# Kernel optimization log

Measured on AMD Instinct MI355X. Metric: run time of the kernel, lower is better.

The kernel has to match this reference:

```python
import jax, jax.numpy as jnp
from jax import lax
import numpy as np

B, H, W = 8, 1024, 1024
NUM_POINTS = 10
THRESHOLD_RATIO = 0.5
K_PEAKS = 512  # cap on peak candidates fed to greedy NMS


def setup_inputs() -> dict:
    key = jax.random.key(0)
    ks = jax.random.split(key, 8)
    return {
        "rgb_image": jax.random.uniform(ks[0], (B, 3, H, W), jnp.float32),
        "depth_image": jax.random.uniform(ks[1], (B, 1, H, W), jnp.float32),
        "conv1_w": jax.random.normal(ks[2], (32, 12, 3, 3), jnp.float32) * 0.1,
        "conv1_b": jax.random.normal(ks[3], (32,), jnp.float32) * 0.1,
        "bn_gamma": jnp.ones((32,), jnp.float32),
        "bn_beta": jnp.zeros((32,), jnp.float32),
        "bn_mean": jax.random.normal(ks[4], (32,), jnp.float32) * 0.1,
        "bn_var": jax.random.uniform(ks[5], (32,), jnp.float32) + 0.5,
        "conv2_w": jax.random.normal(ks[6], (1, 32, 1, 1), jnp.float32) * 0.1,
        "conv2_b": jnp.zeros((1,), jnp.float32),
    }


def dwt2(x):
    # Haar DWT exactly as in the torch module (row split then column split)
    x01 = x[..., 0::2, :] * 0.5
    x02 = x[..., 1::2, :] * 0.5
    LL = x01[..., 0::2] + x02[..., 0::2]
    LH = x01[..., 0::2] - x02[..., 0::2]
    HL = x01[..., 1::2] + x02[..., 1::2]
    HH = x01[..., 1::2] - x02[..., 1::2]
    return LL, LH, HL, HH


def conv2d(x, w, b=None, pad=0, groups=1):
    y = lax.conv_general_dilated(x, w, (1, 1), [(pad, pad), (pad, pad)],
                                 dimension_numbers=("NCHW", "OIHW", "NCHW"),
                                 feature_group_count=groups)
    if b is not None:
        y = y + b[None, :, None, None]
    return y


def gaussian_smooth(x, k=5, sigma=1.0):
    ax = jnp.arange(-(k // 2), k // 2 + 1, dtype=jnp.float32)
    xx, yy = jnp.meshgrid(ax, ax, indexing="ij")
    ker = jnp.exp(-(xx ** 2 + yy ** 2) / (2.0 * sigma ** 2))
    ker = ker / ker.sum()
    C = x.shape[1]
    wk = jnp.tile(ker[None, None], (C, 1, 1, 1))  # depthwise
    return conv2d(x, wk, pad=k // 2, groups=C)


def find_points(s):
    """Greedy spatial-NMS peak picking on a single (h,w) saliency map.
    Returns (NUM_POINTS, 2) normalized (x, y) coords."""
    h, w = s.shape
    min_dist = float(max(max(h, w) // 20, 20))
    flat = s.reshape(-1)
    mp = lax.reduce_window(s, -jnp.inf, lax.max, (3, 3), (1, 1), [(1, 1), (1, 1)])
    peak_flat = ((s == mp) & (s > 0)).reshape(-1)
    peak_scores = jnp.where(peak_flat, flat, -jnp.inf)
    top_vals, top_idx = lax.top_k(peak_scores, K_PEAKS)  # sorted desc = torch argsort
    valid = top_vals > -jnp.inf
    px = (top_idx % w).astype(jnp.float32)
    py = (top_idx // w).astype(jnp.float32)
    pc = jnp.stack([px, py], axis=-1)                     # (K,2)
    dist = jnp.sqrt(((pc[:, None, :] - pc[None, :, :]) ** 2).sum(-1))  # (K,K)
    ar = jnp.arange(K_PEAKS)

    def body(i, st):
        avail, sel, cnt = st
        take = avail[i] & valid[i] & (cnt < NUM_POINTS)
        sel = sel.at[i].set(take)
        suppress = (dist[i] < min_dist) & (ar > i)  # nearby[:i+1]=False in torch
        avail = jnp.where(take, avail & (~suppress), avail)
        return avail, sel, cnt + take.astype(jnp.int32)

    _, sel, n_chosen = lax.fori_loop(
        0, K_PEAKS, body,
        (jnp.ones(K_PEAKS, bool), jnp.zeros(K_PEAKS, bool), jnp.int32(0)))

    # compact chosen peak indices (in descending-score order) into first slots
    pos = jnp.cumsum(sel.astype(jnp.int32)) - 1
    scatter_pos = jnp.where(sel, pos, NUM_POINTS)  # out-of-range -> dropped
    buf = jnp.zeros(NUM_POINTS, jnp.int32).at[scatter_pos].set(top_idx, mode="drop")
    # fallback: top saliency excluding all peaks (matches torch fill-up branch)
    fb_scores = jnp.where(peak_flat, -jnp.inf, flat)
    _, fb_idx = lax.top_k(fb_scores, NUM_POINTS)
    slot = jnp.arange(NUM_POINTS)
    fb = fb_idx[jnp.clip(slot - n_chosen, 0, NUM_POINTS - 1)]
    sel_idx = jnp.where(slot < n_chosen, buf, fb)
    cx = (sel_idx % w).astype(jnp.float32) / w
    cy = (sel_idx // w).astype(jnp.float32) / h
    return jnp.stack([cx, cy], axis=-1)


def boxes_from_mask(masks):
    binm = masks[:, 0] > THRESHOLD_RATIO  # (B,H,W)
    Hh, Ww = binm.shape[1], binm.shape[2]
    rows = binm.any(axis=2)
    cols = binm.any(axis=1)
    ri = jnp.arange(Hh)
    ci = jnp.arange(Ww)
    rmin = jnp.min(jnp.where(rows, ri[None, :], Hh), axis=1)
    rmax = jnp.max(jnp.where(rows, ri[None, :], -1), axis=1)
    cmin = jnp.min(jnp.where(cols, ci[None, :], Ww), axis=1)
    cmax = jnp.max(jnp.where(cols, ci[None, :], -1), axis=1)
    has = rows.any(axis=1)
    boxes = jnp.stack([cmin, rmin, cmax, rmax], axis=-1).astype(jnp.float32)
    default = jnp.array([0.0, 0.0, Ww - 1.0, Hh - 1.0], jnp.float32)
    return jnp.where(has[:, None], boxes, default[None, :])


def reference(rgb_image, depth_image, conv1_w, conv1_b, bn_gamma, bn_beta,
              bn_mean, bn_var, conv2_w, conv2_b):
    rgb_gray = rgb_image.mean(axis=1, keepdims=True)
    rLL, rLH, rHL, rHH = dwt2(rgb_gray)
    dLL, dLH, dHL, dHH = dwt2(depth_image)
    E_rgb = jnp.sqrt(rLH ** 2 + rHL ** 2 + rHH ** 2 + 1e-8)
    E_depth = jnp.sqrt(dLH ** 2 + dHL ** 2 + dHH ** 2 + 1e-8)
    E_rgb_s = gaussian_smooth(E_rgb)
    E_depth_s = gaussian_smooth(E_depth)
    freq = jnp.concatenate(
        [rLL, rLH, rHL, rHH, dLL, dLH, dHL, dHH, E_rgb, E_depth, E_rgb_s, E_depth_s],
        axis=1)  # (B,12,H/2,W/2)
    x = conv2d(freq, conv1_w, conv1_b, pad=1)
    inv = lax.rsqrt(bn_var + 1e-5)
    x = bn_gamma[None, :, None, None] * (x - bn_mean[None, :, None, None]) * inv[None, :, None, None] + bn_beta[None, :, None, None]
    x = jax.nn.gelu(x)
    sal = jax.nn.sigmoid(conv2d(x, conv2_w, conv2_b))  # (B,1,H/2,W/2)
    masks = jax.image.resize(sal, (sal.shape[0], 1, H, W), method="bilinear")
    coords = jax.vmap(find_points)(sal[:, 0])          # (B,N,2)
    labels = jnp.ones((sal.shape[0], NUM_POINTS), jnp.int32)
    boxes = boxes_from_mask(masks)                     # (B,4)
    return coords, labels, boxes, masks
```

## Files before the change

kernel.cpp:

```cpp
#include <hip/hip_runtime.h>
#include <math.h>


#define CHW 262144
#define FULLHW 1048576
#define NB1 64
#define NB2 32
#define PROW 514
#define PREC (514*514)

typedef __attribute__((ext_vector_type(8))) short bf16x8;
typedef __attribute__((ext_vector_type(16))) float f32x16;

static __device__ __forceinline__ unsigned short f2bf(float x) {
  unsigned u = __float_as_uint(x);
  u += 0x7FFFu + ((u >> 16) & 1u);
  return (unsigned short)(u >> 16);
}
static __device__ __forceinline__ float bf2f(unsigned short h) {
  return __uint_as_float(((unsigned)h) << 16);
}

static constexpr size_t OFF_SAL   = 0;
static constexpr size_t OFF_THR   = 8388608;
static constexpr size_t OFF_CNT   = OFF_THR + 256;
static constexpr size_t OFF_CAND  = OFF_CNT + 256;
static constexpr size_t OFF_PART  = OFF_CAND + 131072;
static constexpr size_t OFF_APACK = OFF_PART + 32768;
static constexpr size_t OFF_EP    = OFF_APACK + 20480;
static constexpr size_t OFF_PKM   = OFF_EP + 512;
static constexpr size_t OFF_DYN   = OFF_PKM + 2097152;

static constexpr int SDY[9] = {-1,-1,-1, 0,0,0, 1,1,1};
static constexpr int SDX[9] = {-1, 0, 1,-1,0,1,-1,0,1};

__global__ void k_init(unsigned* __restrict__ cnt,
                       const float* __restrict__ w1, const float* __restrict__ b1,
                       const float* __restrict__ gam, const float* __restrict__ bet,
                       const float* __restrict__ mean, const float* __restrict__ var,
                       const float* __restrict__ w2, const float* __restrict__ b2,
                       unsigned short* __restrict__ apack, float* __restrict__ ep) {
  int i = blockIdx.x * 256 + threadIdx.x;
  if (i < 16) cnt[i] = 0;
  if (i < 9216) {
    int e = i & 7, lane = (i >> 3) & 63, frag = i >> 9;
    int s = frag >> 1, hh = frag & 1;
    int co = lane & 31;
    int c = ((lane >> 5) << 3) + e;
    float val = (c < 12) ? w1[co * 108 + c * 9 + s] : 0.0f;
    unsigned short hb = f2bf(val);
    apack[i] = hh ? f2bf(val - bf2f(hb)) : hb;
  }
  if (i < 96) {
    int t = i >> 5, rem = i & 31, kg = rem >> 4, reg = rem & 15;
    int co = (reg & 3) + 8 * (reg >> 2) + 4 * kg;
    float sc = gam[co] * rsqrtf(var[co] + 1e-5f);
    float v = (t == 0) ? sc
            : (t == 1) ? (b1[co] - mean[co]) * sc + bet[co]
                       : w2[co];
    ep[i] = v;
  } else if (i == 96) {
    ep[96] = b2[0];
  }
}

__global__ __launch_bounds__(256) void k_zero(unsigned short* __restrict__ freq2) {
  int i = blockIdx.x * 256 + threadIdx.x;
  int bi = blockIdx.y;
  if (i >= 8208) return;
  int q = i & 1, r = (i >> 1) % 2052, pl = (i >> 1) / 2052;
  int row, col;
  if (r < 514)        { row = 0;   col = r; }
  else if (r < 1028)  { row = 513; col = r - 514; }
  else if (r < 1540)  { row = r - 1028 + 1; col = 0; }
  else                { row = r - 1540 + 1; col = 513; }
  size_t off = ((size_t)(bi * 2 + pl) * PREC + (size_t)row * PROW + col) * 16;
  uint4* p = (uint4*)(freq2 + off) + q;
  *p = make_uint4(0u, 0u, 0u, 0u);
}

__global__ __launch_bounds__(256) void k_freq(const float* __restrict__ rgb,
                                              const float* __restrict__ dep,
                                              unsigned short* __restrict__ freq2,
                                              float* __restrict__ ebuf, int b0) {
  int t = blockIdx.x * 256 + threadIdx.x;
  int bi = blockIdx.y;
  int b = b0 + bi;
  int xp = t & 255, y = t >> 8;
  const float* base = rgb + (size_t)b * 3 * FULLHW + (size_t)(2 * y) * 1024 + 4 * xp;
  float4 R0 = *(const float4*)(base);
  float4 R1 = *(const float4*)(base + 1024);
  float4 G0 = *(const float4*)(base + FULLHW);
  float4 G1 = *(const float4*)(base + FULLHW + 1024);
  float4 Bl0 = *(const float4*)(base + 2 * FULLHW);
  float4 Bl1 = *(const float4*)(base + 2 * FULLHW + 1024);
  const float* dbase = dep + (size_t)b * FULLHW + (size_t)(2 * y) * 1024 + 4 * xp;
  float4 D0 = *(const float4*)(dbase);
  float4 D1 = *(const float4*)(dbase + 1024);

  float gt[4], gb[4], dt[4], db_[4];
  gt[0] = (R0.x + G0.x + Bl0.x) / 3.0f; gt[1] = (R0.y + G0.y + Bl0.y) / 3.0f;
  gt[2] = (R0.z + G0.z + Bl0.z) / 3.0f; gt[3] = (R0.w + G0.w + Bl0.w) / 3.0f;
  gb[0] = (R1.x + G1.x + Bl1.x) / 3.0f; gb[1] = (R1.y + G1.y + Bl1.y) / 3.0f;
  gb[2] = (R1.z + G1.z + Bl1.z) / 3.0f; gb[3] = (R1.w + G1.w + Bl1.w) / 3.0f;
  dt[0] = D0.x; dt[1] = D0.y; dt[2] = D0.z; dt[3] = D0.w;
  db_[0] = D1.x; db_[1] = D1.y; db_[2] = D1.z; db_[3] = D1.w;

  unsigned short hs[2][8], ls[2][8];
  float er[2], ed[2];
  #pragma unroll
  for (int j = 0; j < 2; ++j) {
    float a = gt[2 * j] * 0.5f, bb = gb[2 * j] * 0.5f;
    float c = gt[2 * j + 1] * 0.5f, d = gb[2 * j + 1] * 0.5f;
    float v[8];
    v[0] = a + bb; v[1] = a - bb; v[2] = c + d; v[3] = c - d;
    float da = dt[2 * j] * 0.5f, db2 = db_[2 * j] * 0.5f;
    float dc = dt[2 * j + 1] * 0.5f, dd = db_[2 * j + 1] * 0.5f;
    v[4] = da + db2; v[5] = da - db2; v[6] = dc + dd; v[7] = dc - dd;
    er[j] = sqrtf(v[1] * v[1] + v[2] * v[2] + v[3] * v[3] + 1e-8f);
    ed[j] = sqrtf(v[5] * v[5] + v[6] * v[6] + v[7] * v[7] + 1e-8f);
    #pragma unroll
    for (int cc = 0; cc < 8; ++cc) {
      unsigned short hb = f2bf(v[cc]);
      hs[j][cc] = hb;
      ls[j][cc] = f2bf(v[cc] - bf2f(hb));
    }
  }
  unsigned short* dst = freq2 +
      ((size_t)(bi * 2) * PREC + (size_t)(y + 1) * PROW + (2 * xp + 1)) * 16;
  uint4* d4 = (uint4*)dst;
  d4[0] = ((const uint4*)hs[0])[0]; d4[1] = ((const uint4*)ls[0])[0];
  d4[2] = ((const uint4*)hs[1])[0]; d4[3] = ((const uint4*)ls[1])[0];
  float* eb = ebuf + (size_t)bi * 2 * CHW + (size_t)y * 512 + 2 * xp;
  *(float2*)(eb) = make_float2(er[0], er[1]);
  *(float2*)(eb + CHW) = make_float2(ed[0], ed[1]);
}

__constant__ float GW[25] = {
  0.00296901f, 0.01330621f, 0.02193824f, 0.01330621f, 0.00296901f,
  0.01330621f, 0.05963435f, 0.09832035f, 0.05963435f, 0.01330621f,
  0.02193824f, 0.09832035f, 0.16210276f, 0.09832035f, 0.02193824f,
  0.01330621f, 0.05963435f, 0.09832035f, 0.05963435f, 0.01330621f,
  0.00296901f, 0.01330621f, 0.02193824f, 0.01330621f, 0.00296901f};

__global__ __launch_bounds__(256) void k_smooth(const float* __restrict__ ebuf,
                                                unsigned short* __restrict__ freq2) {
  int t = blockIdx.x * 256 + threadIdx.x;
  int bi = blockIdx.y;
  int x = t & 511, y = t >> 9;
  const float* eb = ebuf + (size_t)bi * 2 * CHW;
  float accv[2];
  #pragma unroll
  for (int ch = 0; ch < 2; ++ch) {
    const float* fin = eb + ch * CHW;
    float acc = 0.0f;
    #pragma unroll
    for (int i = 0; i < 5; ++i) {
      int yy = y + i - 2;
      if (yy < 0 || yy > 511) continue;
      #pragma unroll
      for (int j = 0; j < 5; ++j) {
        int xx = x + j - 2;
        if (xx < 0 || xx > 511) continue;
        acc += GW[i * 5 + j] * fin[yy * 512 + xx];
      }
    }
    accv[ch] = acc;
  }
  float erc = eb[t], edc = eb[CHW + t];
  unsigned short rec[16];
  float v4[4] = {erc, edc, accv[0], accv[1]};
  #pragma unroll
  for (int j = 0; j < 4; ++j) {
    unsigned short hb = f2bf(v4[j]);
    rec[j] = hb;
    rec[8 + j] = f2bf(v4[j] - bf2f(hb));
  }
  #pragma unroll
  for (int j = 4; j < 8; ++j) { rec[j] = 0; rec[8 + j] = 0; }
  unsigned short* px = freq2 +
      ((size_t)(bi * 2 + 1) * PREC + (size_t)(y + 1) * PROW + (x + 1)) * 16;
  ((uint4*)px)[0] = ((const uint4*)rec)[0];
  ((uint4*)px)[1] = ((const uint4*)rec)[1];
}

__global__ __launch_bounds__(256) void k_conv(const unsigned short* __restrict__ freq2,
    const unsigned short* __restrict__ apack, const float* __restrict__ ep,
    float* __restrict__ sal, int b0) {
  int tid = threadIdx.x;
  int l = tid & 63, wv = tid >> 6;
  int y = blockIdx.y;
  int xw = blockIdx.x * 128 + wv * 32;
  int bi = blockIdx.z;
  int n = l & 31, kg = l >> 5;

  const unsigned short* pb0 = freq2 +
      ((size_t)(bi * 2 + kg) * PREC + (size_t)(y + 1) * PROW + (xw + n + 1)) * 16;
  const unsigned short* ab = apack + l * 8;

  bf16x8 Bh[9], Bl[9];
  #pragma unroll
  for (int s = 0; s < 9; ++s) {
    const int doff = (SDY[s] * PROW + SDX[s]) * 16;
    Bh[s] = *(const bf16x8*)(pb0 + doff);
    Bl[s] = *(const bf16x8*)(pb0 + doff + 8);
  }

  f32x16 acc = {};
  #pragma unroll
  for (int s = 0; s < 9; ++s) {
    bf16x8 Ah = *(const bf16x8*)(ab + s * 1024);
    bf16x8 Al = *(const bf16x8*)(ab + s * 1024 + 512);
    acc = __builtin_amdgcn_mfma_f32_32x32x16_bf16(Ah, Bh[s], acc, 0, 0, 0);
    acc = __builtin_amdgcn_mfma_f32_32x32x16_bf16(Al, Bh[s], acc, 0, 0, 0);
    acc = __builtin_amdgcn_mfma_f32_32x32x16_bf16(Ah, Bl[s], acc, 0, 0, 0);
  }

  const float* e0 = ep + kg * 16;
  const float* e1 = ep + 32 + kg * 16;
  const float* e2 = ep + 64 + kg * 16;
  float s2 = 0.0f;
  #pragma unroll
  for (int r = 0; r < 16; ++r) {
    float t = acc[r] * e0[r] + e1[r];
    float z = t * (1.5957691216057308f + 0.07135481283247183f * (t * t));
    s2 += (t / (1.0f + __expf(-z))) * e2[r];
  }
  s2 += __shfl_xor(s2, 32);
  s2 += ep[96];
  float res = 1.0f / (1.0f + __expf(-s2));
  if (l < 32)
    sal[(size_t)(b0 + bi) * CHW + (size_t)y * 512 + xw + n] = res;
}

__global__ __launch_bounds__(256) void k_resize(const float* __restrict__ sal,
                                                float* __restrict__ masks,
                                                int* __restrict__ part) {
  int b = blockIdx.y;
  int blk = blockIdx.x;
  int t = threadIdx.x;
  const float* sp = sal + (size_t)b * CHW;
  float* mp = masks + (size_t)b * FULLHW;
  int mnX = 0x7FFFFFFF, mxX = -1, mnY = 0x7FFFFFFF, mxY = -1;
  int c0 = 4 * t;
  #pragma unroll
  for (int r = 0; r < 4; ++r) {
    int Y = blk * 4 + r;
    int y0 = (Y - 1) >> 1;
    float wy = (Y & 1) ? 0.25f : 0.75f;
    int y0c = y0 < 0 ? 0 : y0, y1c = (y0 + 1 > 511) ? 511 : y0 + 1;
    const float* r0 = sp + y0c * 512;
    const float* r1 = sp + y1c * 512;
    float o[4];
    #pragma unroll
    for (int j = 0; j < 4; ++j) {
      int X = c0 + j;
      int x0 = (X - 1) >> 1;
      float wx = (X & 1) ? 0.25f : 0.75f;
      int x0c = x0 < 0 ? 0 : x0, x1c = (x0 + 1 > 511) ? 511 : x0 + 1;
      float v00 = r0[x0c], v01 = r0[x1c], v10 = r1[x0c], v11 = r1[x1c];
      o[j] = (1.0f - wy) * ((1.0f - wx) * v00 + wx * v01)
           + wy * ((1.0f - wx) * v10 + wx * v11);
      if (o[j] > 0.5f) {
        mnX = min(mnX, X); mxX = max(mxX, X);
        mnY = min(mnY, Y); mxY = max(mxY, Y);
      }
    }
    *(float4*)(mp + (size_t)Y * 1024 + c0) = make_float4(o[0], o[1], o[2], o[3]);
  }
  __shared__ int s0[256], s1[256], s2[256], s3[256];
  s0[t] = mnX; s1[t] = mxX; s2[t] = mnY; s3[t] = mxY;
  __syncthreads();
  for (int off = 128; off > 0; off >>= 1) {
    if (t < off) {
      s0[t] = min(s0[t], s0[t + off]); s1[t] = max(s1[t], s1[t + off]);
      s2[t] = min(s2[t], s2[t + off]); s3[t] = max(s3[t], s3[t + off]);
    }
    __syncthreads();
  }
  if (t == 0) {
    int* pp = part + (b * 256 + blk) * 4;
    pp[0] = s0[0]; pp[1] = s1[0]; pp[2] = s2[0]; pp[3] = s3[0];
  }
}

__global__ __launch_bounds__(256) void k_boxreduce(const int* __restrict__ part,
                                                   float* __restrict__ out) {
  int b = blockIdx.x, t = threadIdx.x;
  const int* pp = part + (b * 256 + t) * 4;
  __shared__ int s0[256], s1[256], s2[256], s3[256];
  s0[t] = pp[0]; s1[t] = pp[1]; s2[t] = pp[2]; s3[t] = pp[3];
  __syncthreads();
  for (int off = 128; off > 0; off >>= 1) {
    if (t < off) {
      s0[t] = min(s0[t], s0[t + off]); s1[t] = max(s1[t], s1[t + off]);
      s2[t] = min(s2[t], s2[t + off]); s3[t] = max(s3[t], s3[t + off]);
    }
    __syncthreads();
  }
  if (t == 0) {
    float x0, y0, x1, y1;
    if (s3[0] < 0) { x0 = 0.0f; y0 = 0.0f; x1 = 1023.0f; y1 = 1023.0f; }
    else { x0 = (float)s0[0]; y0 = (float)s2[0]; x1 = (float)s1[0]; y1 = (float)s3[0]; }
    out[240 + b * 4 + 0] = x0;
    out[240 + b * 4 + 1] = y0;
    out[240 + b * 4 + 2] = x1;
    out[240 + b * 4 + 3] = y1;
  }
}

__global__ __launch_bounds__(256) void k_hist1(const float* __restrict__ sal,
                                               unsigned* __restrict__ h1p,
                                               unsigned char* __restrict__ pkm) {
  __shared__ unsigned sH[4096];
  int b = blockIdx.y, tid = threadIdx.x;
  for (int i = tid; i < 4096; i += 256) sH[i] = 0;
  __syncthreads();
  const float* sp = sal + (size_t)b * CHW;
  int base = blockIdx.x * 4096;
  for (int it = 0; it < 4; ++it) {
    int p = base + it * 1024 + tid * 4;
    int x0 = p & 511, y = p >> 9;
    int ym = (y > 0) ? y - 1 : 0, yp = (y < 511) ? y + 1 : 511;
    const float* r0 = sp + ym * 512;
    const float* r1 = sp + y * 512;
    const float* r2 = sp + yp * 512;
    float4 m0 = *(const float4*)(r0 + x0);
    float4 m1 = *(const float4*)(r1 + x0);
    float4 m2 = *(const float4*)(r2 + x0);
    float l0 = x0 ? r0[x0 - 1] : m0.x;
    float l1 = x0 ? r1[x0 - 1] : m1.x;
    float l2 = x0 ? r2[x0 - 1] : m2.x;
    float q0 = (x0 < 508) ? r0[x0 + 4] : m0.w;
    float q1 = (x0 < 508) ? r1[x0 + 4] : m1.w;
    float q2 = (x0 < 508) ? r2[x0 + 4] : m2.w;
    float a0[6] = {l0, m0.x, m0.y, m0.z, m0.w, q0};
    float a1[6] = {l1, m1.x, m1.y, m1.z, m1.w, q1};
    float a2[6] = {l2, m2.x, m2.y, m2.z, m2.w, q2};
    unsigned pw = 0;
    #pragma unroll
    for (int j = 0; j < 4; ++j) {
      float r0m = fmaxf(fmaxf(a0[j], a0[j + 1]), a0[j + 2]);
      float r1m = fmaxf(fmaxf(a1[j], a1[j + 1]), a1[j + 2]);
      float r2m = fmaxf(fmaxf(a2[j], a2[j + 1]), a2[j + 2]);
      float cmax = fmaxf(fmaxf(r0m, r1m), r2m);
      float sv = a1[j + 1];
      bool pk = (sv > 0.0f) && (sv >= cmax);
      pw |= (pk ? 1u : 0u) << (8 * j);
      unsigned bin = (__float_as_uint(sv) >> 21) & 2047;
      atomicAdd(&sH[(pk ? 0 : 2048) + bin], 1u);
    }
    *(unsigned*)(pkm + (size_t)b * CHW + p) = pw;
  }
  __syncthreads();
  unsigned* dst = h1p + ((size_t)b * NB1 + blockIdx.x) * 4096;
  for (int i = tid; i < 4096; i += 256) dst[i] = sH[i];
}

__global__ __launch_bounds__(256) void k_scan(const unsigned* __restrict__ hp,
                                              int* __restrict__ thr, int level,
                                              int np) {
  int c = blockIdx.x, b = blockIdx.y, t = threadIdx.x;
  __shared__ unsigned sBins[2048];
  __shared__ unsigned sS[256];
  __shared__ int sT;
  unsigned bv[8] = {0, 0, 0, 0, 0, 0, 0, 0};
  for (int p = 0; p < np; ++p) {
    const unsigned* q = hp + ((size_t)(b * np + p)) * 4096 + c * 2048 + t * 8;
    uint4 a = *(const uint4*)(q);
    uint4 d = *(const uint4*)(q + 4);
    bv[0] += a.x; bv[1] += a.y; bv[2] += a.z; bv[3] += a.w;
    bv[4] += d.x; bv[5] += d.y; bv[6] += d.z; bv[7] += d.w;
  }
  unsigned part = 0;
  #pragma unroll
  for (int r = 0; r < 8; ++r) {
    sBins[t * 8 + r] = bv[r];
    part += bv[r];
  }
  sS[t] = part;
  __syncthreads();
  for (int off = 1; off < 256; off <<= 1) {
    unsigned add = (t + off < 256) ? sS[t + off] : 0;
    __syncthreads();
    sS[t] += add;
    __syncthreads();
  }
  int K = (c == 0) ? 512 : 10;
  int* tb = thr + (c * 8 + b) * 4;
  if (level == 1) { K -= tb[1]; if (K < 1) K = 1; }
  if (t == 0) sT = -1;
  __syncthreads();
  if (sS[t] >= (unsigned)K && (t == 255 || sS[t + 1] < (unsigned)K)) sT = t;
  __syncthreads();
  if (t == 0) {
    int T = 0;
    unsigned run = 0;
    if (sT >= 0) {
      int ts = sT;
      run = (ts < 255) ? sS[ts + 1] : 0;
      for (int r = 7; r >= 0; --r) {
        unsigned v = sBins[ts * 8 + r];
        run += v;
        if (run >= (unsigned)K) { T = ts * 8 + r; run -= v; break; }
      }
    } else {
      T = 0;
      run = sS[0] - sBins[0];
    }
    if (level == 0) { tb[0] = T; tb[1] = (int)run; }
    else           { tb[2] = (tb[0] << 11) | T; }
  }
}

__global__ __launch_bounds__(256) void k_hist2(const float* __restrict__ sal,
                                               const unsigned char* __restrict__ pkm,
                                               const int* __restrict__ thr,
                                               unsigned* __restrict__ h2p) {
  __shared__ unsigned sH[4096];
  int b = blockIdx.y, tid = threadIdx.x;
  for (int i = tid; i < 4096; i += 256) sH[i] = 0;
  __syncthreads();
  int t0 = thr[(0 * 8 + b) * 4];
  int t1 = thr[(1 * 8 + b) * 4];
  const float* sp = sal + (size_t)b * CHW;
  const unsigned char* pp = pkm + (size_t)b * CHW;
  int base = blockIdx.x * 8192;
  for (int it = 0; it < 8; ++it) {
    int p = base + it * 1024 + tid * 4;
    float4 s4 = *(const float4*)(sp + p);
    unsigned pk4 = *(const unsigned*)(pp + p);
    float sv[4] = {s4.x, s4.y, s4.z, s4.w};
    #pragma unroll
    for (int j = 0; j < 4; ++j) {
      bool pk = ((pk4 >> (8 * j)) & 255u) != 0;
      unsigned bits = __float_as_uint(sv[j]);
      int tt = pk ? t0 : t1;
      if ((int)(bits >> 21) == tt)
        atomicAdd(&sH[(pk ? 0 : 2048) + ((bits >> 10) & 2047)], 1u);
    }
  }
  __syncthreads();
  unsigned* dst = h2p + ((size_t)b * NB2 + blockIdx.x) * 4096;
  for (int i = tid; i < 4096; i += 256) dst[i] = sH[i];
}

__global__ __launch_bounds__(256) void k_compact(const float* __restrict__ sal,
                                                 const unsigned char* __restrict__ pkm,
                                                 const int* __restrict__ thr,
                                                 unsigned* __restrict__ cnt,
                                                 unsigned long long* __restrict__ cand) {
  int b = blockIdx.y;
  int p = (blockIdx.x * 256 + threadIdx.x) * 4;
  const float* sp = sal + (size_t)b * CHW;
  float4 s4 = *(const float4*)(sp + p);
  unsigned pk4 = *(const unsigned*)(pkm + (size_t)b * CHW + p);
  unsigned q0 = (unsigned)thr[(0 * 8 + b) * 4 + 2];
  unsigned q1 = (unsigned)thr[(1 * 8 + b) * 4 + 2];
  float sv[4] = {s4.x, s4.y, s4.z, s4.w};
  #pragma unroll
  for (int j = 0; j < 4; ++j) {
    bool pk = ((pk4 >> (8 * j)) & 255u) != 0;
    unsigned bits = __float_as_uint(sv[j]);
    unsigned q = pk ? q0 : q1;
    int c = pk ? 0 : 1;
    if ((bits >> 10) >= q) {
      unsigned pos = atomicAdd(&cnt[c * 8 + b], 1u);
      if (pos < 1024)
        cand[((size_t)(c * 8 + b) << 10) + pos] =
            ((unsigned long long)bits << 32) | (unsigned)(~(p + j));
    }
  }
}

__device__ inline void bitonic1024_desc(unsigned long long* sKey) {
  int t = threadIdx.x;
  for (unsigned k = 2; k <= 1024; k <<= 1) {
    for (unsigned j = k >> 1; j > 0; j >>= 1) {
      __syncthreads();
      #pragma unroll
      for (int e = 0; e < 2; ++e) {
        unsigned i = (unsigned)t + (unsigned)e * 512u;
        unsigned l = i ^ j;
        if (l > i) {
          unsigned long long a = sKey[i], bb = sKey[l];
          if (((i & k) == 0) ? (a < bb) : (a > bb)) { sKey[i] = bb; sKey[l] = a; }
        }
      }
    }
  }
  __syncthreads();
}

__global__ __launch_bounds__(512) void k_nms(const unsigned long long* __restrict__ cand,
                                             const unsigned* __restrict__ cnt,
                                             float* __restrict__ out) {
  __shared__ unsigned long long sKey[1024];
  __shared__ unsigned sIdx[512];
  __shared__ int sAvail[512];
  __shared__ int sSel[16];
  int b = blockIdx.x, t = threadIdx.x;
  if (t < 10) out[160 + b * 10 + t] = 1.0f;
  int Cp = (int)cnt[b]; if (Cp > 1024) Cp = 1024;
  const unsigned long long* cp = cand + ((size_t)b << 10);
  sKey[t] = (t < Cp) ? cp[t] : 0ULL;
  sKey[t + 512] = (t + 512 < Cp) ? cp[t + 512] : 0ULL;
  bitonic1024_desc(sKey);
  sIdx[t] = (unsigned)(~sKey[t]);
  int ncand = (Cp < 512) ? Cp : 512;
  sAvail[t] = (t < ncand) ? 1 : 0;
  __syncthreads();
  int nsel = 0;
  for (int i = 0; i < 512 && nsel < 10; ++i) {
    if (sAvail[i] != 0) {
      unsigned pi = sIdx[i];
      int xi = (int)(pi & 511), yi = (int)(pi >> 9);
      if (t > i && sAvail[t]) {
        int dx = (int)(sIdx[t] & 511) - xi;
        int dy = (int)(sIdx[t] >> 9) - yi;
        if (dx * dx + dy * dy < 625) sAvail[t] = 0;
      }
      if (t == 0) sSel[nsel] = (int)pi;
      ++nsel;
      __syncthreads();
    }
  }
  __syncthreads();
  int Cf = (int)cnt[8 + b]; if (Cf > 1024) Cf = 1024;
  const unsigned long long* cf = cand + ((size_t)(8 + b) << 10);
  sKey[t] = (t < Cf) ? cf[t] : 0ULL;
  sKey[t + 512] = (t + 512 < Cf) ? cf[t + 512] : 0ULL;
  bitonic1024_desc(sKey);
  if (t < 10) {
    int fi;
    if (t < nsel) fi = sSel[t];
    else { int r = t - nsel; if (r > 9) r = 9; fi = (int)((unsigned)(~sKey[r])); }
    out[((size_t)b * 10 + t) * 2 + 0] = (float)(fi & 511) * (1.0f / 512.0f);
    out[((size_t)b * 10 + t) * 2 + 1] = (float)(fi >> 9) * (1.0f / 512.0f);
  }
}

extern "C" void kernel_launch(void* const* d_in, const int* in_sizes, int n_in,
                              void* d_out, int out_size, void* d_ws, size_t ws_size,
                              hipStream_t stream) {
  const float* rgb  = (const float*)d_in[0];
  const float* dep  = (const float*)d_in[1];
  const float* w1   = (const float*)d_in[2];
  const float* b1   = (const float*)d_in[3];
  const float* gam  = (const float*)d_in[4];
  const float* bet  = (const float*)d_in[5];
  const float* bmn  = (const float*)d_in[6];
  const float* bvr  = (const float*)d_in[7];
  const float* w2   = (const float*)d_in[8];
  const float* b2   = (const float*)d_in[9];
  float* out = (float*)d_out;
  char* ws = (char*)d_ws;

  float* sal = (float*)(ws + OFF_SAL);
  int* thr = (int*)(ws + OFF_THR);
  unsigned* cnt = (unsigned*)(ws + OFF_CNT);
  unsigned long long* cand = (unsigned long long*)(ws + OFF_CAND);
  int* part = (int*)(ws + OFF_PART);
  unsigned short* apack = (unsigned short*)(ws + OFF_APACK);
  float* ep = (float*)(ws + OFF_EP);
  unsigned char* pkm = (unsigned char*)(ws + OFF_PKM);

  size_t perE = (size_t)2 * CHW * 4;
  size_t perF = (size_t)PREC * 64;
  long long avail = (long long)ws_size - (long long)OFF_DYN;
  int nb = 1;
  if (avail >= (long long)(perE + perF)) {
    long long m = avail / (long long)(perE + perF);
    nb = (m > 8) ? 8 : (int)m;
  }
  float* ebuf = (float*)(ws + OFF_DYN);
  unsigned short* freq2 = (unsigned short*)(ws + OFF_DYN + perE * (size_t)nb);
  unsigned* h1p = (unsigned*)(ws + OFF_DYN);
  unsigned* h2p = (unsigned*)(ws + OFF_DYN + (size_t)8 * NB1 * 4096 * 4);

  k_init<<<40, 256, 0, stream>>>(cnt, w1, b1, gam, bet, bmn, bvr, w2, b2,
                                 apack, ep);
  k_zero<<<dim3(33, nb), 256, 0, stream>>>(freq2);

  for (int b0 = 0; b0 < 8; b0 += nb) {
    int nbc = (8 - b0 < nb) ? (8 - b0) : nb;
    k_freq<<<dim3(512, nbc), 256, 0, stream>>>(rgb, dep, freq2, ebuf, b0);
    k_smooth<<<dim3(1024, nbc), 256, 0, stream>>>(ebuf, freq2);
    k_conv<<<dim3(4, 512, nbc), 256, 0, stream>>>(freq2, apack, ep, sal, b0);
  }

  k_resize<<<dim3(256, 8), 256, 0, stream>>>(sal, out + 272, part);
  k_boxreduce<<<8, 256, 0, stream>>>(part, out);
  k_hist1<<<dim3(NB1, 8), 256, 0, stream>>>(sal, h1p, pkm);
  k_scan<<<dim3(2, 8), 256, 0, stream>>>(h1p, thr, 0, NB1);
  k_hist2<<<dim3(NB2, 8), 256, 0, stream>>>(sal, pkm, thr, h2p);
  k_scan<<<dim3(2, 8), 256, 0, stream>>>(h2p, thr, 1, NB2);
  k_compact<<<dim3(256, 8), 256, 0, stream>>>(sal, pkm, thr, cnt, cand);
  k_nms<<<8, 512, 0, stream>>>(cand, cnt, out);
}
```

Baseline: 524.1 us.

## Stage conv input halo in LDS with planar hi/lo bf16 layout

The padded frequency buffer changes from interleaved 16-short records per pixel (hi and lo together) to four planes of 8 shorts each, split into hi and lo for two channel groups. The conv kernel now loads a 3-row by 130-column halo tile for all four planes into shared memory once per block. The nine 3x3 taps are then read from LDS instead of issuing 18 overlapping global loads per lane. The GELU and sigmoid divisions are also replaced by hardware reciprocal approximations. This trades extra LDS traffic, a block barrier and a small accuracy loss for less redundant global and L2 traffic.

```diff
diff --git a/kernel.cpp b/kernel.cpp
--- a/kernel.cpp
+++ b/kernel.cpp
@@ -8,6 +8,7 @@
 #define NB2 32
 #define PROW 514
 #define PREC (514*514)
+#define LREC 130
 
 typedef __attribute__((ext_vector_type(8))) short bf16x8;
 typedef __attribute__((ext_vector_type(16))) float f32x16;
@@ -68,14 +69,13 @@
   int i = blockIdx.x * 256 + threadIdx.x;
   int bi = blockIdx.y;
   if (i >= 8208) return;
-  int q = i & 1, r = (i >> 1) % 2052, pl = (i >> 1) / 2052;
+  int pl = i / 2052, r = i % 2052;
   int row, col;
   if (r < 514)        { row = 0;   col = r; }
   else if (r < 1028)  { row = 513; col = r - 514; }
   else if (r < 1540)  { row = r - 1028 + 1; col = 0; }
   else                { row = r - 1540 + 1; col = 513; }
-  size_t off = ((size_t)(bi * 2 + pl) * PREC + (size_t)row * PROW + col) * 16;
-  uint4* p = (uint4*)(freq2 + off) + q;
+  uint4* p = (uint4*)(freq2 + ((size_t)(bi * 4 + pl) * PREC + (size_t)row * PROW + col) * 8);
   *p = make_uint4(0u, 0u, 0u, 0u);
 }
 
@@ -126,11 +126,13 @@
       ls[j][cc] = f2bf(v[cc] - bf2f(hb));
     }
   }
-  unsigned short* dst = freq2 +
-      ((size_t)(bi * 2) * PREC + (size_t)(y + 1) * PROW + (2 * xp + 1)) * 16;
-  uint4* d4 = (uint4*)dst;
-  d4[0] = ((const uint4*)hs[0])[0]; d4[1] = ((const uint4*)ls[0])[0];
-  d4[2] = ((const uint4*)hs[1])[0]; d4[3] = ((const uint4*)ls[1])[0];
+  size_t rbase = (size_t)(y + 1) * PROW + (2 * xp + 1);
+  unsigned short* d0 = freq2 + ((size_t)(bi * 4 + 0) * PREC + rbase) * 8;
+  unsigned short* d1 = freq2 + ((size_t)(bi * 4 + 1) * PREC + rbase) * 8;
+  ((uint4*)d0)[0] = ((const uint4*)hs[0])[0];
+  ((uint4*)d0)[1] = ((const uint4*)hs[1])[0];
+  ((uint4*)d1)[0] = ((const uint4*)ls[0])[0];
+  ((uint4*)d1)[1] = ((const uint4*)ls[1])[0];
   float* eb = ebuf + (size_t)bi * 2 * CHW + (size_t)y * 512 + 2 * xp;
   *(float2*)(eb) = make_float2(er[0], er[1]);
   *(float2*)(eb + CHW) = make_float2(ed[0], ed[1]);
@@ -168,52 +170,62 @@
     accv[ch] = acc;
   }
   float erc = eb[t], edc = eb[CHW + t];
-  unsigned short rec[16];
+  unsigned short rh[8], rl[8];
   float v4[4] = {erc, edc, accv[0], accv[1]};
   #pragma unroll
   for (int j = 0; j < 4; ++j) {
     unsigned short hb = f2bf(v4[j]);
-    rec[j] = hb;
-    rec[8 + j] = f2bf(v4[j] - bf2f(hb));
-  }
-  #pragma unroll
-  for (int j = 4; j < 8; ++j) { rec[j] = 0; rec[8 + j] = 0; }
-  unsigned short* px = freq2 +
-      ((size_t)(bi * 2 + 1) * PREC + (size_t)(y + 1) * PROW + (x + 1)) * 16;
-  ((uint4*)px)[0] = ((const uint4*)rec)[0];
-  ((uint4*)px)[1] = ((const uint4*)rec)[1];
+    rh[j] = hb;
+    rl[j] = f2bf(v4[j] - bf2f(hb));
+  }
+  #pragma unroll
+  for (int j = 4; j < 8; ++j) { rh[j] = 0; rl[j] = 0; }
+  size_t rbase = (size_t)(y + 1) * PROW + (x + 1);
+  unsigned short* p2 = freq2 + ((size_t)(bi * 4 + 2) * PREC + rbase) * 8;
+  unsigned short* p3 = freq2 + ((size_t)(bi * 4 + 3) * PREC + rbase) * 8;
+  *(uint4*)p2 = *(const uint4*)rh;
+  *(uint4*)p3 = *(const uint4*)rl;
 }
 
 __global__ __launch_bounds__(256) void k_conv(const unsigned short* __restrict__ freq2,
     const unsigned short* __restrict__ apack, const float* __restrict__ ep,
     float* __restrict__ sal, int b0) {
+  __shared__ __align__(16) char smem[24960];
   int tid = threadIdx.x;
   int l = tid & 63, wv = tid >> 6;
   int y = blockIdx.y;
-  int xw = blockIdx.x * 128 + wv * 32;
+  int xwb = blockIdx.x * 128;
   int bi = blockIdx.z;
   int n = l & 31, kg = l >> 5;
 
-  const unsigned short* pb0 = freq2 +
-      ((size_t)(bi * 2 + kg) * PREC + (size_t)(y + 1) * PROW + (xw + n + 1)) * 16;
+  #pragma unroll
+  for (int it = 0; it < 7; ++it) {
+    int j = it * 256 + tid;
+    if (j < 1560) {
+      int row = j / 520, rem = j % 520;
+      int plane = rem / 130, rec = rem % 130;
+      const unsigned short* g = freq2 +
+          ((size_t)(bi * 4 + plane) * PREC + (size_t)(y + row) * PROW + (xwb + rec)) * 8;
+      *(uint4*)(smem + j * 16) = *(const uint4*)g;
+    }
+  }
+  __syncthreads();
+
   const unsigned short* ab = apack + l * 8;
-
-  bf16x8 Bh[9], Bl[9];
+  f32x16 acc = {};
   #pragma unroll
   for (int s = 0; s < 9; ++s) {
-    const int doff = (SDY[s] * PROW + SDX[s]) * 16;
-    Bh[s] = *(const bf16x8*)(pb0 + doff);
-    Bl[s] = *(const bf16x8*)(pb0 + doff + 8);
-  }
-
-  f32x16 acc = {};
-  #pragma unroll
-  for (int s = 0; s < 9; ++s) {
+    int row = 1 + SDY[s];
+    int rec = wv * 32 + n + 1 + SDX[s];
+    const char* bh = smem + (((row * 4 + kg * 2 + 0) * LREC) + rec) * 16;
+    const char* bl = smem + (((row * 4 + kg * 2 + 1) * LREC) + rec) * 16;
+    bf16x8 Bh = *(const bf16x8*)bh;
+    bf16x8 Bl = *(const bf16x8*)bl;
     bf16x8 Ah = *(const bf16x8*)(ab + s * 1024);
     bf16x8 Al = *(const bf16x8*)(ab + s * 1024 + 512);
-    acc = __builtin_amdgcn_mfma_f32_32x32x16_bf16(Ah, Bh[s], acc, 0, 0, 0);
-    acc = __builtin_amdgcn_mfma_f32_32x32x16_bf16(Al, Bh[s], acc, 0, 0, 0);
-    acc = __builtin_amdgcn_mfma_f32_32x32x16_bf16(Ah, Bl[s], acc, 0, 0, 0);
+    acc = __builtin_amdgcn_mfma_f32_32x32x16_bf16(Ah, Bh, acc, 0, 0, 0);
+    acc = __builtin_amdgcn_mfma_f32_32x32x16_bf16(Al, Bh, acc, 0, 0, 0);
+    acc = __builtin_amdgcn_mfma_f32_32x32x16_bf16(Ah, Bl, acc, 0, 0, 0);
   }
 
   const float* e0 = ep + kg * 16;
@@ -224,13 +236,14 @@
   for (int r = 0; r < 16; ++r) {
     float t = acc[r] * e0[r] + e1[r];
     float z = t * (1.5957691216057308f + 0.07135481283247183f * (t * t));
-    s2 += (t / (1.0f + __expf(-z))) * e2[r];
+    float g = t * __builtin_amdgcn_rcpf(1.0f + __expf(-z));
+    s2 += g * e2[r];
   }
   s2 += __shfl_xor(s2, 32);
   s2 += ep[96];
-  float res = 1.0f / (1.0f + __expf(-s2));
+  float res = __builtin_amdgcn_rcpf(1.0f + __expf(-s2));
   if (l < 32)
-    sal[(size_t)(b0 + bi) * CHW + (size_t)y * 512 + xw + n] = res;
+    sal[(size_t)(b0 + bi) * CHW + (size_t)y * 512 + xwb + wv * 32 + n] = res;
 }
 
 __global__ __launch_bounds__(256) void k_resize(const float* __restrict__ sal,
```

New measurement: 509.8 us. -2.7%, faster.
